# Kernel tuning notes

Hardware: AMD Instinct MI355X
Metric: run time of the kernel (lower is better)

The kernel has to match this reference:

```python
import jax, jax.numpy as jnp
import numpy as np

N_ATOMS = 100_000
N_PAIRS = 3_200_000


def setup_inputs() -> dict:
    key = jax.random.key(0)
    k0, k1, k2, k3, k4 = jax.random.split(key, 5)
    atomic_numbers = jax.random.randint(k0, (N_ATOMS,), 1, 95, dtype=jnp.int32)
    distances = jax.random.uniform(k1, (N_PAIRS,), jnp.float32, 0.5, 5.0)
    cutoffs = jax.random.uniform(k2, (N_PAIRS,), jnp.float32)
    idx_i = jnp.sort(jax.random.randint(k3, (N_PAIRS,), 0, N_ATOMS, dtype=jnp.int32))
    idx_j = jax.random.randint(k4, (N_PAIRS,), 0, N_ATOMS, dtype=jnp.int32)
    # ZBL parameters (trainable=True defaults from __init__)
    a_coefficient = jnp.array([0.8854], dtype=jnp.float32)
    a_exponent = jnp.array([0.23], dtype=jnp.float32)
    phi_coefficients = jnp.array([0.18175, 0.50986, 0.28022, 0.02817], dtype=jnp.float32)
    phi_exponents = jnp.array([3.1998, 0.94229, 0.4029, 0.20162], dtype=jnp.float32)
    # unit conversion buffers: identity units -> factors = 1.0
    ke = jnp.array([1.0 / (4.0 * np.pi * 0.005526349406)], dtype=jnp.float32)
    distances_model2Ang = jnp.array([1.0], dtype=jnp.float32)
    energies_Hatree2model = jnp.array([1.0], dtype=jnp.float32)
    return dict(atomic_numbers=atomic_numbers, distances=distances, cutoffs=cutoffs,
                idx_i=idx_i, idx_j=idx_j, a_coefficient=a_coefficient,
                a_exponent=a_exponent, phi_coefficients=phi_coefficients,
                phi_exponents=phi_exponents, ke=ke,
                distances_model2Ang=distances_model2Ang,
                energies_Hatree2model=energies_Hatree2model)


def reference(atomic_numbers, distances, cutoffs, idx_i, idx_j,
              a_coefficient, a_exponent, phi_coefficients, phi_exponents,
              ke, distances_model2Ang, energies_Hatree2model):
    Z = atomic_numbers.astype(distances.dtype)            # [N]
    distances_ang = distances * distances_model2Ang        # [P]
    za = Z ** jnp.abs(a_exponent)                          # [N] (a_exponent is [1])
    a_ij = jnp.abs(a_coefficient) / (za[idx_i] + za[idx_j])  # [P]
    arguments = distances / a_ij                           # [P] (faithful: uses model-unit distances)
    # L1-normalized |phi_coefficients|
    abs_c = jnp.abs(phi_coefficients)
    coefficients = abs_c / jnp.sum(abs_c)                  # [4]
    exponents = jnp.abs(phi_exponents)                     # [4]
    # phi[p] = sum_k c_k * exp(-e_k * arg_p)  -> [P,4] intermediate
    phi = jnp.sum(coefficients[None, :] * jnp.exp(-exponents[None, :] * arguments[:, None]), axis=1)
    repulsion = ke * Z[idx_i] * Z[idx_j] / distances_ang * phi * cutoffs  # [P]
    Erep = energies_Hatree2model * jax.ops.segment_sum(repulsion, idx_i, num_segments=N_ATOMS)
    return Erep
```

## Files before the change

### kernel.cpp

```cpp
#include <hip/hip_runtime.h>
#include <math.h>

#define LOG2E 1.4426950408889634f

__global__ void __launch_bounds__(256)
zbl_prep(const int* __restrict__ Z, unsigned char* __restrict__ z8,
         float* __restrict__ out, int n_atoms, int out_n) {
    int i = blockIdx.x * blockDim.x + threadIdx.x;
    if (i < n_atoms) z8[i] = (unsigned char)Z[i];
    if (i < out_n)   out[i] = 0.0f;
}

__global__ void __launch_bounds__(256)
zbl_pairs8(const float* __restrict__ dist, const float* __restrict__ cut,
           const int* __restrict__ idx_i, const int* __restrict__ idx_j,
           const unsigned char* __restrict__ z8,
           const float* __restrict__ a_coef, const float* __restrict__ a_exp,
           const float* __restrict__ phi_c, const float* __restrict__ phi_e,
           const float* __restrict__ ke, const float* __restrict__ d2a,
           const float* __restrict__ e2m,
           float* __restrict__ out, int n) {
    __shared__ float za_tab[128];

    float aexp   = fabsf(a_exp[0]);
    float inv_ac = __fdividef(1.0f, fabsf(a_coef[0]));
    float c0 = fabsf(phi_c[0]), c1 = fabsf(phi_c[1]),
          c2 = fabsf(phi_c[2]), c3 = fabsf(phi_c[3]);
    float cnorm = __fdividef(1.0f, c0 + c1 + c2 + c3);
    c0 *= cnorm; c1 *= cnorm; c2 *= cnorm; c3 *= cnorm;
    float e0 = fabsf(phi_e[0]) * LOG2E, e1 = fabsf(phi_e[1]) * LOG2E,
          e2 = fabsf(phi_e[2]) * LOG2E, e3 = fabsf(phi_e[3]) * LOG2E;
    float scale = ke[0] * e2m[0] * __fdividef(1.0f, d2a[0]);

    int t = threadIdx.x;
    if (t < 128) za_tab[t] = (t >= 1) ? exp2f(aexp * __log2f((float)t)) : 0.0f;
    __syncthreads();

    int gid = blockIdx.x * blockDim.x + t;
    int p0  = gid * 8;

    int   k[8];
    float v[8];

    if (p0 + 7 < n) {
        const float4* dist4 = (const float4*)dist;
        const float4* cut4  = (const float4*)cut;
        const int4*   ii4   = (const int4*)idx_i;
        const int4*   jj4   = (const int4*)idx_j;
        float4 dA = dist4[2 * gid], dB = dist4[2 * gid + 1];
        float4 cA = cut4[2 * gid],  cB = cut4[2 * gid + 1];
        int4   iA = ii4[2 * gid],   iB = ii4[2 * gid + 1];
        int4   jA = jj4[2 * gid],   jB = jj4[2 * gid + 1];

        k[0] = iA.x; k[1] = iA.y; k[2] = iA.z; k[3] = iA.w;
        k[4] = iB.x; k[5] = iB.y; k[6] = iB.z; k[7] = iB.w;
        int j[8] = { jA.x, jA.y, jA.z, jA.w, jB.x, jB.y, jB.z, jB.w };
        float d[8]  = { dA.x, dA.y, dA.z, dA.w, dB.x, dB.y, dB.z, dB.w };
        float cu[8] = { cA.x, cA.y, cA.z, cA.w, cB.x, cB.y, cB.z, cB.w };

        int zi[8], zj[8];
        #pragma unroll
        for (int q = 0; q < 8; ++q) zi[q] = (int)z8[k[q]];
        #pragma unroll
        for (int q = 0; q < 8; ++q) zj[q] = (int)z8[j[q]];

        #pragma unroll
        for (int q = 0; q < 8; ++q) {
            float arg = d[q] * (za_tab[zi[q]] + za_tab[zj[q]]) * inv_ac;
            float phi = c0 * exp2f(-e0 * arg) + c1 * exp2f(-e1 * arg)
                      + c2 * exp2f(-e2 * arg) + c3 * exp2f(-e3 * arg);
            v[q] = scale * (float)(zi[q] * zj[q]) * phi * cu[q]
                 * __fdividef(1.0f, d[q]);
        }
    } else {
        #pragma unroll
        for (int q = 0; q < 8; ++q) {
            int p = p0 + q;
            if (p < n) {
                int ki = idx_i[p], jj = idx_j[p];
                int zi = (int)z8[ki], zj = (int)z8[jj];
                float dd = dist[p];
                float arg = dd * (za_tab[zi] + za_tab[zj]) * inv_ac;
                float phi = c0 * exp2f(-e0 * arg) + c1 * exp2f(-e1 * arg)
                          + c2 * exp2f(-e2 * arg) + c3 * exp2f(-e3 * arg);
                k[q] = ki;
                v[q] = scale * (float)(zi * zj) * phi * cut[p]
                     * __fdividef(1.0f, dd);
            } else {
                k[q] = (q > 0) ? k[q - 1] : -1;
                v[q] = 0.0f;
            }
        }
    }

    float run = v[0];
    float firstRun = 0.0f;
    bool  firstEnds = false;
    int   runStart = 0;
    #pragma unroll
    for (int q = 1; q < 8; ++q) {
        if (k[q] == k[q - 1]) {
            run += v[q];
        } else {
            if (runStart == 0) { firstRun = run; firstEnds = true; }
            else if (k[q - 1] >= 0) atomicAdd(out + k[q - 1], run);
            run = v[q];
            runStart = q;
        }
    }
    float c   = run;
    int   key = k[7];

    int lane = t & 63;
    #pragma unroll
    for (int off = 1; off < 64; off <<= 1) {
        float ov = __shfl_up(c, (unsigned)off, 64);
        int   ok = __shfl_up(key, (unsigned)off, 64);
        if (lane >= off && ok == key) c += ov;
    }

    float prev_c   = __shfl_up(c, 1u, 64);
    int   prev_key = __shfl_up(key, 1u, 64);
    int   next_k0  = __shfl_down(k[0], 1u, 64);

    if (k[0] >= 0 && firstEnds) {
        float tot = firstRun + ((lane > 0 && prev_key == k[0]) ? prev_c : 0.0f);
        atomicAdd(out + k[0], tot);
    }
    bool tail = (lane == 63) || (next_k0 != key);
    if (key >= 0 && tail) atomicAdd(out + key, c);
}

extern "C" void kernel_launch(void* const* d_in, const int* in_sizes, int n_in,
                              void* d_out, int out_size, void* d_ws, size_t ws_size,
                              hipStream_t stream) {
    const int*   atomic_numbers = (const int*)  d_in[0];
    const float* distances      = (const float*)d_in[1];
    const float* cutoffs        = (const float*)d_in[2];
    const int*   idx_i          = (const int*)  d_in[3];
    const int*   idx_j          = (const int*)  d_in[4];
    const float* a_coefficient  = (const float*)d_in[5];
    const float* a_exponent     = (const float*)d_in[6];
    const float* phi_coeffs     = (const float*)d_in[7];
    const float* phi_exps       = (const float*)d_in[8];
    const float* ke             = (const float*)d_in[9];
    const float* d2a            = (const float*)d_in[10];
    const float* e2m            = (const float*)d_in[11];
    float* out = (float*)d_out;

    const int n_atoms = in_sizes[0];
    const int n_pairs = in_sizes[1];

    const int block = 256;
    const int n_threads = (n_pairs + 7) / 8;
    const int grid_pairs = (n_threads + block - 1) / block;
    const int grid_prep  = (((n_atoms > out_size) ? n_atoms : out_size) + block - 1) / block;

    unsigned char* z8 = (unsigned char*)d_ws;
    zbl_prep<<<grid_prep, block, 0, stream>>>(
        atomic_numbers, z8, out, n_atoms, out_size);
    zbl_pairs8<<<grid_pairs, block, 0, stream>>>(
        distances, cutoffs, idx_i, idx_j, z8,
        a_coefficient, a_exponent, phi_coeffs, phi_exps, ke, d2a, e2m,
        out, n_pairs);
}
```

Measured before the change: 117.4 us.

## Stage the atomic-number byte table in LDS with a persistent 256-block grid

Adds a kernel that copies the whole 100K-entry uint8 atomic-number table into dynamic shared memory once per block. Pair gathers for Z[i] and Z[j] then read LDS instead of global or L2, and 256 blocks of 1024 threads each loop over a contiguous chunk of pairs. This removes the random global gathers but adds about 100KB of table copy per block (256 copies in total). It also leaves one large block per CU, which limits occupancy and latency hiding. It falls back to the old kernel when the table does not fit in LDS.

Result: no change. 118.4 us (+0.9%).

```diff
diff --git a/kernel.cpp b/kernel.cpp
--- a/kernel.cpp
+++ b/kernel.cpp
@@ -9,6 +9,144 @@
     int i = blockIdx.x * blockDim.x + threadIdx.x;
     if (i < n_atoms) z8[i] = (unsigned char)Z[i];
     if (i < out_n)   out[i] = 0.0f;
+}
+
+__global__ void __launch_bounds__(1024)
+zbl_pairs_lds(const float* __restrict__ dist, const float* __restrict__ cut,
+              const int* __restrict__ idx_i, const int* __restrict__ idx_j,
+              const unsigned char* __restrict__ z8,
+              const float* __restrict__ a_coef, const float* __restrict__ a_exp,
+              const float* __restrict__ phi_c, const float* __restrict__ phi_e,
+              const float* __restrict__ ke, const float* __restrict__ d2a,
+              const float* __restrict__ e2m,
+              float* __restrict__ out, int n, int n_atoms, int per_block) {
+    __shared__ float za_tab[128];
+    extern __shared__ unsigned char z8s[];
+
+    float aexp   = fabsf(a_exp[0]);
+    float inv_ac = __fdividef(1.0f, fabsf(a_coef[0]));
+    float c0 = fabsf(phi_c[0]), c1 = fabsf(phi_c[1]),
+          c2 = fabsf(phi_c[2]), c3 = fabsf(phi_c[3]);
+    float cnorm = __fdividef(1.0f, c0 + c1 + c2 + c3);
+    c0 *= cnorm; c1 *= cnorm; c2 *= cnorm; c3 *= cnorm;
+    float e0 = fabsf(phi_e[0]) * LOG2E, e1 = fabsf(phi_e[1]) * LOG2E,
+          e2 = fabsf(phi_e[2]) * LOG2E, e3 = fabsf(phi_e[3]) * LOG2E;
+    float scale = ke[0] * e2m[0] * __fdividef(1.0f, d2a[0]);
+
+    int t = threadIdx.x;
+
+    int start = blockIdx.x * per_block;
+    int end   = (start + per_block < n) ? (start + per_block) : n;
+    if (start >= end) return;
+
+    if (t < 128) za_tab[t] = (t >= 1) ? exp2f(aexp * __log2f((float)t)) : 0.0f;
+
+    {
+        const unsigned int* src = (const unsigned int*)z8;
+        unsigned int*       dst = (unsigned int*)z8s;
+        int nw = n_atoms >> 2;
+        for (int w = t; w < nw; w += blockDim.x) dst[w] = src[w];
+        int rem = n_atoms & 3;
+        if (t < rem) z8s[(nw << 2) + t] = z8[(nw << 2) + t];
+    }
+    __syncthreads();
+
+    int lane = t & 63;
+
+    for (int pb = start; pb < end; pb += blockDim.x * 8) {
+        int p0 = pb + t * 8;
+
+        int   k[8];
+        float v[8];
+
+        if (p0 + 7 < end) {
+            int w4 = p0 >> 2;
+            const float4* dist4 = (const float4*)dist;
+            const float4* cut4  = (const float4*)cut;
+            const int4*   ii4   = (const int4*)idx_i;
+            const int4*   jj4   = (const int4*)idx_j;
+            float4 dA = dist4[w4], dB = dist4[w4 + 1];
+            float4 cA = cut4[w4],  cB = cut4[w4 + 1];
+            int4   iA = ii4[w4],   iB = ii4[w4 + 1];
+            int4   jA = jj4[w4],   jB = jj4[w4 + 1];
+
+            k[0] = iA.x; k[1] = iA.y; k[2] = iA.z; k[3] = iA.w;
+            k[4] = iB.x; k[5] = iB.y; k[6] = iB.z; k[7] = iB.w;
+            int j[8] = { jA.x, jA.y, jA.z, jA.w, jB.x, jB.y, jB.z, jB.w };
+            float d[8]  = { dA.x, dA.y, dA.z, dA.w, dB.x, dB.y, dB.z, dB.w };
+            float cu[8] = { cA.x, cA.y, cA.z, cA.w, cB.x, cB.y, cB.z, cB.w };
+
+            int zi[8], zj[8];
+            #pragma unroll
+            for (int q = 0; q < 8; ++q) zi[q] = (int)z8s[k[q]];
+            #pragma unroll
+            for (int q = 0; q < 8; ++q) zj[q] = (int)z8s[j[q]];
+
+            #pragma unroll
+            for (int q = 0; q < 8; ++q) {
+                float arg = d[q] * (za_tab[zi[q]] + za_tab[zj[q]]) * inv_ac;
+                float phi = c0 * exp2f(-e0 * arg) + c1 * exp2f(-e1 * arg)
+                          + c2 * exp2f(-e2 * arg) + c3 * exp2f(-e3 * arg);
+                v[q] = scale * (float)(zi[q] * zj[q]) * phi * cu[q]
+                     * __fdividef(1.0f, d[q]);
+            }
+        } else {
+            #pragma unroll
+            for (int q = 0; q < 8; ++q) {
+                int p = p0 + q;
+                if (p < end) {
+                    int ki = idx_i[p], jj = idx_j[p];
+                    int zi = (int)z8s[ki], zj = (int)z8s[jj];
+                    float dd = dist[p];
+                    float arg = dd * (za_tab[zi] + za_tab[zj]) * inv_ac;
+                    float phi = c0 * exp2f(-e0 * arg) + c1 * exp2f(-e1 * arg)
+                              + c2 * exp2f(-e2 * arg) + c3 * exp2f(-e3 * arg);
+                    k[q] = ki;
+                    v[q] = scale * (float)(zi * zj) * phi * cut[p]
+                         * __fdividef(1.0f, dd);
+                } else {
+                    k[q] = (q > 0) ? k[q - 1] : -1;
+                    v[q] = 0.0f;
+                }
+            }
+        }
+
+        float run = v[0];
+        float firstRun = 0.0f;
+        bool  firstEnds = false;
+        int   runStart = 0;
+        #pragma unroll
+        for (int q = 1; q < 8; ++q) {
+            if (k[q] == k[q - 1]) {
+                run += v[q];
+            } else {
+                if (runStart == 0) { firstRun = run; firstEnds = true; }
+                else if (k[q - 1] >= 0) atomicAdd(out + k[q - 1], run);
+                run = v[q];
+                runStart = q;
+            }
+        }
+        float c   = run;
+        int   key = k[7];
+
+        #pragma unroll
+        for (int off = 1; off < 64; off <<= 1) {
+            float ov = __shfl_up(c, (unsigned)off, 64);
+            int   ok = __shfl_up(key, (unsigned)off, 64);
+            if (lane >= off && ok == key) c += ov;
+        }
+
+        float prev_c   = __shfl_up(c, 1u, 64);
+        int   prev_key = __shfl_up(key, 1u, 64);
+        int   next_k0  = __shfl_down(k[0], 1u, 64);
+
+        if (k[0] >= 0 && firstEnds) {
+            float tot = firstRun + ((lane > 0 && prev_key == k[0]) ? prev_c : 0.0f);
+            atomicAdd(out + k[0], tot);
+        }
+        bool tail = (lane == 63) || (next_k0 != key);
+        if (key >= 0 && tail) atomicAdd(out + key, c);
+    }
 }
 
 __global__ void __launch_bounds__(256)
@@ -152,15 +290,26 @@
     const int n_pairs = in_sizes[1];
 
     const int block = 256;
-    const int n_threads = (n_pairs + 7) / 8;
-    const int grid_pairs = (n_threads + block - 1) / block;
-    const int grid_prep  = (((n_atoms > out_size) ? n_atoms : out_size) + block - 1) / block;
+    const int grid_prep = (((n_atoms > out_size) ? n_atoms : out_size) + block - 1) / block;
 
     unsigned char* z8 = (unsigned char*)d_ws;
     zbl_prep<<<grid_prep, block, 0, stream>>>(
         atomic_numbers, z8, out, n_atoms, out_size);
-    zbl_pairs8<<<grid_pairs, block, 0, stream>>>(
-        distances, cutoffs, idx_i, idx_j, z8,
-        a_coefficient, a_exponent, phi_coeffs, phi_exps, ke, d2a, e2m,
-        out, n_pairs);
+
+    if (n_atoms + 1024 <= 150 * 1024) {
+        const int pblock = 1024;
+        const int grid   = 256;
+        int per_block = ((n_pairs + grid * 8 - 1) / (grid * 8)) * 8;
+        zbl_pairs_lds<<<grid, pblock, (size_t)n_atoms, stream>>>(
+            distances, cutoffs, idx_i, idx_j, z8,
+            a_coefficient, a_exponent, phi_coeffs, phi_exps, ke, d2a, e2m,
+            out, n_pairs, n_atoms, per_block);
+    } else {
+        const int n_threads  = (n_pairs + 7) / 8;
+        const int grid_pairs = (n_threads + block - 1) / block;
+        zbl_pairs8<<<grid_pairs, block, 0, stream>>>(
+            distances, cutoffs, idx_i, idx_j, z8,
+            a_coefficient, a_exponent, phi_coeffs, phi_exps, ke, d2a, e2m,
+            out, n_pairs);
+    }
 }
```
